# Kernel tuning notes

Hardware: AMD Instinct MI355X
Metric: run time of the kernel (lower is better)

## Reference

```python
import jax, jax.numpy as jnp
import numpy as np

NUM_CLUSTERS = 32
EPS = 1e-12

def _l2norm(v, axis):
    return v / jnp.maximum(jnp.linalg.norm(v, axis=axis, keepdims=True), EPS)

def setup_inputs() -> dict:
    key = jax.random.key(0)
    k1, k2, k3 = jax.random.split(key, 3)
    B, M, D, K = 64, 512, 2048, NUM_CLUSTERS
    init_sc = 1.0 / np.sqrt(D)
    x = jax.random.normal(k1, (B, M, D), dtype=jnp.float32)
    W = init_sc * jax.random.normal(k2, (K, D), dtype=jnp.float32)
    centroids = init_sc * jax.random.normal(k3, (K, D), dtype=jnp.float32)
    return {"x": x, "W": W, "centroids": centroids}

def reference(x, W, centroids):
    # x: [B, M, D] frame features; W: [K, D]; centroids: [K, D]
    xn = _l2norm(x, axis=-1)                              # per-frame L2 normalize
    sa = jax.nn.softmax(jnp.einsum('bmd,kd->bmk', xn, W), axis=-1)  # [B, M, K]
    # vlad[b,k,d] = sum_m sa[b,m,k] * (xn[b,m,d] - centroids[k,d])
    #            = (sa^T @ xn)[b,k,d] - colsum(sa)[b,k] * centroids[k,d]
    agg = jnp.einsum('bmk,bmd->bkd', sa, xn)              # [B, K, D]
    vlad = agg - jnp.sum(sa, axis=1)[..., None] * centroids[None]
    vlad = _l2norm(vlad, axis=2)                          # intra-normalize per cluster
    vlad = vlad.reshape(vlad.shape[0], -1)                # [B, K*D]
    return _l2norm(vlad, axis=1)
```

## Files before the change

kernel.cpp:

```cpp
#include <hip/hip_runtime.h>
#include <hip/hip_bf16.h>
#include <cstdint>
#include <cstddef>

#define Bn 64
#define Mn 512
#define Dn 2048
#define Kn 32
#define EPSF 1e-12f

typedef __attribute__((ext_vector_type(8))) __bf16 bf16x8;
typedef __attribute__((ext_vector_type(4))) __bf16 bf16x4;
typedef __attribute__((ext_vector_type(4))) float f32x4;

__global__ __launch_bounds__(256) void k0_prep(const float* __restrict__ W,
                                               __bf16* __restrict__ Wb,
                                               float* __restrict__ ssq) {
  int idx = blockIdx.x * 256 + threadIdx.x;
  if (idx < Kn * Dn) Wb[idx] = (__bf16)W[idx];
  if (idx < Bn * Kn) ssq[idx] = 0.f;
}

__global__ __launch_bounds__(256) void k1_logits(const float* __restrict__ x,
                                                 const __bf16* __restrict__ Wb,
                                                 float* __restrict__ logits,
                                                 float* __restrict__ invn) {
  int wv = threadIdx.x >> 6, lane = threadIdx.x & 63;
  int mr = lane & 15, q = lane >> 4;
  int row0 = (blockIdx.x * 4 + wv) * 16;
  const float* xp = x + (size_t)(row0 + mr) * Dn + q * 8;
  const __bf16* wp = Wb + (size_t)mr * Dn + q * 8;
  f32x4 acc0 = {0.f, 0.f, 0.f, 0.f};
  f32x4 acc1 = {0.f, 0.f, 0.f, 0.f};
  float ssq = 0.f;
#pragma unroll 2
  for (int s = 0; s < 64; ++s) {
    f32x4 xa = *(const f32x4*)(xp + s * 32);
    f32x4 xb = *(const f32x4*)(xp + s * 32 + 4);
    bf16x8 af;
    af[0] = (__bf16)xa[0]; af[1] = (__bf16)xa[1];
    af[2] = (__bf16)xa[2]; af[3] = (__bf16)xa[3];
    af[4] = (__bf16)xb[0]; af[5] = (__bf16)xb[1];
    af[6] = (__bf16)xb[2]; af[7] = (__bf16)xb[3];
    ssq = fmaf(xa[0], xa[0], ssq); ssq = fmaf(xa[1], xa[1], ssq);
    ssq = fmaf(xa[2], xa[2], ssq); ssq = fmaf(xa[3], xa[3], ssq);
    ssq = fmaf(xb[0], xb[0], ssq); ssq = fmaf(xb[1], xb[1], ssq);
    ssq = fmaf(xb[2], xb[2], ssq); ssq = fmaf(xb[3], xb[3], ssq);
    bf16x8 b0 = *(const bf16x8*)(wp + s * 32);
    bf16x8 b1 = *(const bf16x8*)(wp + (size_t)16 * Dn + s * 32);
    acc0 = __builtin_amdgcn_mfma_f32_16x16x32_bf16(af, b0, acc0, 0, 0, 0);
    acc1 = __builtin_amdgcn_mfma_f32_16x16x32_bf16(af, b1, acc1, 0, 0, 0);
  }
#pragma unroll
  for (int r = 0; r < 4; ++r) {
    int row = row0 + q * 4 + r;
    logits[(size_t)row * Kn + mr] = acc0[r];
    logits[(size_t)row * Kn + mr + 16] = acc1[r];
  }
  ssq += __shfl_xor(ssq, 16);
  ssq += __shfl_xor(ssq, 32);
  if (lane < 16) invn[row0 + lane] = 1.f / fmaxf(sqrtf(ssq), EPSF);
}

__global__ __launch_bounds__(512) void k2_softmax(const float* __restrict__ logits,
                                                  const float* __restrict__ invn,
                                                  __bf16* __restrict__ sapT,
                                                  float* __restrict__ colsum) {
  __shared__ float csw[8][Kn + 1];
  int b = blockIdx.x, t = threadIdx.x;
  int row = b * Mn + t;
  float inv = invn[row];
  const float* lp = logits + (size_t)row * Kn;
  float v[Kn];
#pragma unroll
  for (int k = 0; k < Kn; ++k) v[k] = lp[k] * inv;
  float mx = v[0];
#pragma unroll
  for (int k = 1; k < Kn; ++k) mx = fmaxf(mx, v[k]);
  float sum = 0.f;
#pragma unroll
  for (int k = 0; k < Kn; ++k) { v[k] = __expf(v[k] - mx); sum += v[k]; }
  float rs = 1.f / sum;
  __bf16* sp = sapT + (size_t)b * (Kn * Mn) + t;
#pragma unroll
  for (int k = 0; k < Kn; ++k) {
    v[k] *= rs;
    sp[(size_t)k * Mn] = (__bf16)(v[k] * inv);
  }
#pragma unroll
  for (int k = 0; k < Kn; ++k) {
#pragma unroll
    for (int off = 1; off <= 32; off <<= 1) v[k] += __shfl_xor(v[k], off);
  }
  int wv = t >> 6, lane = t & 63;
#pragma unroll
  for (int k = 0; k < Kn; ++k)
    if (lane == k) csw[wv][k] = v[k];
  __syncthreads();
  if (t < Kn) {
    float s = 0.f;
#pragma unroll
    for (int w = 0; w < 8; ++w) s += csw[w][t];
    colsum[b * Kn + t] = s;
  }
}

#define XS 36
#define AS 520
__global__ __launch_bounds__(256) void k3_agg(const float* __restrict__ x,
                                              const __bf16* __restrict__ sapT,
                                              const float* __restrict__ colsum,
                                              const float* __restrict__ cent,
                                              float* __restrict__ vlad,
                                              float* __restrict__ ssq) {
  __shared__ __bf16 xT[256 * XS];
  __shared__ __bf16 saT[Kn * AS];
  __shared__ float csl[Kn];
  int b = blockIdx.x >> 3;
  int dchunk = (blockIdx.x & 7) * 256;
  int t = threadIdx.x;
  {
    const __bf16* sg = sapT + (size_t)b * (Kn * Mn);
#pragma unroll
    for (int i = 0; i < 8; ++i) {
      int f = t + 256 * i;
      int k = f >> 6;
      int mg = (f & 63) * 8;
      *(bf16x8*)&saT[k * AS + mg] = *(const bf16x8*)(sg + k * Mn + mg);
    }
    if (t < Kn) csl[t] = colsum[b * Kn + t];
  }
  int w = t >> 6, lane = t & 63;
  int mr = lane & 15, q = lane >> 4;
  int r_ = t >> 3, qq = t & 7;
  const float* xg = x + (size_t)b * Mn * Dn + dchunk;
  f32x4 acc[2][4] = {};
  for (int m0 = 0; m0 < Mn; m0 += 32) {
    __syncthreads();
#pragma unroll
    for (int i = 0; i < 8; ++i) {
      int c0 = (qq + 8 * i) * 4;
      f32x4 xv = *(const f32x4*)(xg + (size_t)(m0 + r_) * Dn + c0);
      xT[(c0 + 0) * XS + r_] = (__bf16)xv[0];
      xT[(c0 + 1) * XS + r_] = (__bf16)xv[1];
      xT[(c0 + 2) * XS + r_] = (__bf16)xv[2];
      xT[(c0 + 3) * XS + r_] = (__bf16)xv[3];
    }
    __syncthreads();
    bf16x8 a0 = *(const bf16x8*)&saT[mr * AS + m0 + q * 8];
    bf16x8 a1 = *(const bf16x8*)&saT[(mr + 16) * AS + m0 + q * 8];
#pragma unroll
    for (int dt = 0; dt < 4; ++dt) {
      int c = w * 64 + dt * 16 + mr;
      bf16x4 lo = *(const bf16x4*)&xT[c * XS + q * 8];
      bf16x4 hi = *(const bf16x4*)&xT[c * XS + q * 8 + 4];
      bf16x8 bv = __builtin_shufflevector(lo, hi, 0, 1, 2, 3, 4, 5, 6, 7);
      acc[0][dt] = __builtin_amdgcn_mfma_f32_16x16x32_bf16(a0, bv, acc[0][dt], 0, 0, 0);
      acc[1][dt] = __builtin_amdgcn_mfma_f32_16x16x32_bf16(a1, bv, acc[1][dt], 0, 0, 0);
    }
  }
#pragma unroll
  for (int kt = 0; kt < 2; ++kt) {
#pragma unroll
    for (int r = 0; r < 4; ++r) {
      int kc = kt * 16 + q * 4 + r;
      float csv = csl[kc];
      float sqa = 0.f;
#pragma unroll
      for (int dt = 0; dt < 4; ++dt) {
        int col = dchunk + w * 64 + dt * 16 + mr;
        float vv = acc[kt][dt][r] - csv * cent[(size_t)kc * Dn + col];
        vlad[((size_t)(b * Kn + kc)) * Dn + col] = vv;
        sqa = fmaf(vv, vv, sqa);
      }
      sqa += __shfl_xor(sqa, 1); sqa += __shfl_xor(sqa, 2);
      sqa += __shfl_xor(sqa, 4); sqa += __shfl_xor(sqa, 8);
      if (mr == 0) atomicAdd(&ssq[b * Kn + kc], sqa);
    }
  }
}

__global__ __launch_bounds__(256) void k4_norm(float* __restrict__ out,
                                               const float* __restrict__ ssq) {
  __shared__ float rk[Kn];
  __shared__ float us[Kn];
  int b = blockIdx.x >> 4;
  int t = threadIdx.x;
  if (t < Kn) {
    float ss = ssq[b * Kn + t];
    float r = 1.f / fmaxf(sqrtf(ss), EPSF);
    rk[t] = r;
    us[t] = ss * r * r;
  }
  __syncthreads();
  float S = 0.f;
#pragma unroll
  for (int k = 0; k < Kn; ++k) S += us[k];
  float s = 1.f / fmaxf(sqrtf(S), EPSF);
  int chunk = blockIdx.x & 15;
  size_t base = (size_t)b * (Kn * Dn) + (size_t)chunk * 4096;
  f32x4* p = (f32x4*)(out + base);
#pragma unroll
  for (int i = 0; i < 4; ++i) {
    int idx = t + 256 * i;
    int k = (chunk * 4096 + idx * 4) >> 11;
    f32x4 v = p[idx];
    float sc = rk[k] * s;
    v[0] *= sc; v[1] *= sc; v[2] *= sc; v[3] *= sc;
    p[idx] = v;
  }
}

extern "C" void kernel_launch(void* const* d_in, const int* in_sizes, int n_in,
                              void* d_out, int out_size, void* d_ws, size_t ws_size,
                              hipStream_t stream) {
  const float* x = (const float*)d_in[0];
  const float* W = (const float*)d_in[1];
  const float* cent = (const float*)d_in[2];
  float* out = (float*)d_out;
  char* ws = (char*)d_ws;
  __bf16* Wb = (__bf16*)ws;
  float* invn = (float*)(ws + (131072));
  __bf16* sapT = (__bf16*)(ws + (262144));
  float* colsum = (float*)(ws + (262144 + 2097152));
  float* ssqb = (float*)(ws + (262144 + 2097152 + 8192));
  float* logits = out;
  hipLaunchKernelGGL(k0_prep, dim3(256), dim3(256), 0, stream, W, Wb, ssqb);
  hipLaunchKernelGGL(k1_logits, dim3(512), dim3(256), 0, stream, x, Wb, logits, invn);
  hipLaunchKernelGGL(k2_softmax, dim3(Bn), dim3(512), 0, stream, logits, invn, sapT, colsum);
  hipLaunchKernelGGL(k3_agg, dim3(512), dim3(256), 0, stream, x, sapT, colsum, cent, out, ssqb);
  hipLaunchKernelGGL(k4_norm, dim3(1024), dim3(256), 0, stream, out, ssqb);
}
```

Measured before the change: 452.7 us.

## Fuse softmax into logits kernel and rewrite aggregation as fp32 FMA

Softmax, its per-row normalization scaling and the cluster column sums now run inside the logits MFMA kernel using lane shuffles, with atomics for the column sums. This removes the separate softmax launch and the logits round-trip through global memory. The aggregation kernel drops the bf16 MFMA path, whose transpose into LDS used scattered bf16 stores. Instead each thread owns one feature column and accumulates 32 clusters with scalar fp32 FMAs against soft-assignment tiles broadcast from LDS. This trades matrix-core throughput and LDS reuse for plain vector ALU work with coalesced x reads, and adds more atomics.

```diff
diff --git a/kernel.cpp b/kernel.cpp
--- a/kernel.cpp
+++ b/kernel.cpp
@@ -10,24 +10,25 @@
 #define EPSF 1e-12f
 
 typedef __attribute__((ext_vector_type(8))) __bf16 bf16x8;
-typedef __attribute__((ext_vector_type(4))) __bf16 bf16x4;
 typedef __attribute__((ext_vector_type(4))) float f32x4;
 
 __global__ __launch_bounds__(256) void k0_prep(const float* __restrict__ W,
                                                __bf16* __restrict__ Wb,
+                                               float* __restrict__ colsum,
                                                float* __restrict__ ssq) {
   int idx = blockIdx.x * 256 + threadIdx.x;
   if (idx < Kn * Dn) Wb[idx] = (__bf16)W[idx];
-  if (idx < Bn * Kn) ssq[idx] = 0.f;
-}
-
-__global__ __launch_bounds__(256) void k1_logits(const float* __restrict__ x,
-                                                 const __bf16* __restrict__ Wb,
-                                                 float* __restrict__ logits,
-                                                 float* __restrict__ invn) {
+  if (idx < Bn * Kn) { colsum[idx] = 0.f; ssq[idx] = 0.f; }
+}
+
+__global__ __launch_bounds__(256) void k1_logits_softmax(const float* __restrict__ x,
+                                                         const __bf16* __restrict__ Wb,
+                                                         __bf16* __restrict__ saP,
+                                                         float* __restrict__ colsum) {
   int wv = threadIdx.x >> 6, lane = threadIdx.x & 63;
   int mr = lane & 15, q = lane >> 4;
   int row0 = (blockIdx.x * 4 + wv) * 16;
+  int b = row0 >> 9;
   const float* xp = x + (size_t)(row0 + mr) * Dn + q * 8;
   const __bf16* wp = Wb + (size_t)mr * Dn + q * 8;
   f32x4 acc0 = {0.f, 0.f, 0.f, 0.f};
@@ -51,132 +52,102 @@
     acc0 = __builtin_amdgcn_mfma_f32_16x16x32_bf16(af, b0, acc0, 0, 0, 0);
     acc1 = __builtin_amdgcn_mfma_f32_16x16x32_bf16(af, b1, acc1, 0, 0, 0);
   }
-#pragma unroll
-  for (int r = 0; r < 4; ++r) {
-    int row = row0 + q * 4 + r;
-    logits[(size_t)row * Kn + mr] = acc0[r];
-    logits[(size_t)row * Kn + mr + 16] = acc1[r];
-  }
   ssq += __shfl_xor(ssq, 16);
   ssq += __shfl_xor(ssq, 32);
-  if (lane < 16) invn[row0 + lane] = 1.f / fmaxf(sqrtf(ssq), EPSF);
-}
-
-__global__ __launch_bounds__(512) void k2_softmax(const float* __restrict__ logits,
-                                                  const float* __restrict__ invn,
-                                                  __bf16* __restrict__ sapT,
-                                                  float* __restrict__ colsum) {
-  __shared__ float csw[8][Kn + 1];
-  int b = blockIdx.x, t = threadIdx.x;
-  int row = b * Mn + t;
-  float inv = invn[row];
-  const float* lp = logits + (size_t)row * Kn;
-  float v[Kn];
-#pragma unroll
-  for (int k = 0; k < Kn; ++k) v[k] = lp[k] * inv;
-  float mx = v[0];
-#pragma unroll
-  for (int k = 1; k < Kn; ++k) mx = fmaxf(mx, v[k]);
-  float sum = 0.f;
-#pragma unroll
-  for (int k = 0; k < Kn; ++k) { v[k] = __expf(v[k] - mx); sum += v[k]; }
-  float rs = 1.f / sum;
-  __bf16* sp = sapT + (size_t)b * (Kn * Mn) + t;
-#pragma unroll
-  for (int k = 0; k < Kn; ++k) {
-    v[k] *= rs;
-    sp[(size_t)k * Mn] = (__bf16)(v[k] * inv);
-  }
-#pragma unroll
-  for (int k = 0; k < Kn; ++k) {
-#pragma unroll
-    for (int off = 1; off <= 32; off <<= 1) v[k] += __shfl_xor(v[k], off);
-  }
-  int wv = t >> 6, lane = t & 63;
-#pragma unroll
-  for (int k = 0; k < Kn; ++k)
-    if (lane == k) csw[wv][k] = v[k];
-  __syncthreads();
-  if (t < Kn) {
-    float s = 0.f;
-#pragma unroll
-    for (int w = 0; w < 8; ++w) s += csw[w][t];
-    colsum[b * Kn + t] = s;
-  }
-}
-
-#define XS 36
-#define AS 520
+  float invb = 1.f / fmaxf(sqrtf(ssq), EPSF);
+  float cs0 = 0.f, cs1 = 0.f;
+#pragma unroll
+  for (int r = 0; r < 4; ++r) {
+    float inv = __shfl(invb, q * 4 + r);
+    float v0 = acc0[r] * inv, v1 = acc1[r] * inv;
+    float mx = fmaxf(v0, v1);
+    mx = fmaxf(mx, __shfl_xor(mx, 1));
+    mx = fmaxf(mx, __shfl_xor(mx, 2));
+    mx = fmaxf(mx, __shfl_xor(mx, 4));
+    mx = fmaxf(mx, __shfl_xor(mx, 8));
+    float e0 = __expf(v0 - mx), e1 = __expf(v1 - mx);
+    float sm = e0 + e1;
+    sm += __shfl_xor(sm, 1); sm += __shfl_xor(sm, 2);
+    sm += __shfl_xor(sm, 4); sm += __shfl_xor(sm, 8);
+    float rs = 1.f / sm;
+    float sa0 = e0 * rs, sa1 = e1 * rs;
+    size_t ro = (size_t)(row0 + q * 4 + r) * Kn;
+    saP[ro + mr]      = (__bf16)(sa0 * inv);
+    saP[ro + mr + 16] = (__bf16)(sa1 * inv);
+    cs0 += sa0; cs1 += sa1;
+  }
+  cs0 += __shfl_xor(cs0, 16); cs0 += __shfl_xor(cs0, 32);
+  cs1 += __shfl_xor(cs1, 16); cs1 += __shfl_xor(cs1, 32);
+  if (lane < 16) {
+    atomicAdd(&colsum[b * Kn + mr], cs0);
+    atomicAdd(&colsum[b * Kn + mr + 16], cs1);
+  }
+}
+
+#define MT 128
 __global__ __launch_bounds__(256) void k3_agg(const float* __restrict__ x,
-                                              const __bf16* __restrict__ sapT,
+                                              const __bf16* __restrict__ saP,
                                               const float* __restrict__ colsum,
                                               const float* __restrict__ cent,
                                               float* __restrict__ vlad,
                                               float* __restrict__ ssq) {
-  __shared__ __bf16 xT[256 * XS];
-  __shared__ __bf16 saT[Kn * AS];
+  __shared__ float sa_t[MT * Kn];
   __shared__ float csl[Kn];
   int b = blockIdx.x >> 3;
-  int dchunk = (blockIdx.x & 7) * 256;
+  int d = (blockIdx.x & 7) * 256 + threadIdx.x;
   int t = threadIdx.x;
-  {
-    const __bf16* sg = sapT + (size_t)b * (Kn * Mn);
-#pragma unroll
-    for (int i = 0; i < 8; ++i) {
-      int f = t + 256 * i;
-      int k = f >> 6;
-      int mg = (f & 63) * 8;
-      *(bf16x8*)&saT[k * AS + mg] = *(const bf16x8*)(sg + k * Mn + mg);
-    }
-    if (t < Kn) csl[t] = colsum[b * Kn + t];
-  }
-  int w = t >> 6, lane = t & 63;
-  int mr = lane & 15, q = lane >> 4;
-  int r_ = t >> 3, qq = t & 7;
-  const float* xg = x + (size_t)b * Mn * Dn + dchunk;
-  f32x4 acc[2][4] = {};
-  for (int m0 = 0; m0 < Mn; m0 += 32) {
+  if (t < Kn) csl[t] = colsum[b * Kn + t];
+  float acc[Kn];
+#pragma unroll
+  for (int k = 0; k < Kn; ++k) acc[k] = 0.f;
+  const float* xb = x + (size_t)b * Mn * Dn + d;
+  const __bf16* sb = saP + (size_t)b * Mn * Kn;
+  for (int mt = 0; mt < Mn; mt += MT) {
     __syncthreads();
 #pragma unroll
-    for (int i = 0; i < 8; ++i) {
-      int c0 = (qq + 8 * i) * 4;
-      f32x4 xv = *(const f32x4*)(xg + (size_t)(m0 + r_) * Dn + c0);
-      xT[(c0 + 0) * XS + r_] = (__bf16)xv[0];
-      xT[(c0 + 1) * XS + r_] = (__bf16)xv[1];
-      xT[(c0 + 2) * XS + r_] = (__bf16)xv[2];
-      xT[(c0 + 3) * XS + r_] = (__bf16)xv[3];
+    for (int i = 0; i < 2; ++i) {
+      int u = t + 256 * i;
+      bf16x8 v8 = *(const bf16x8*)(sb + (size_t)(mt)*Kn + (size_t)u * 8);
+#pragma unroll
+      for (int j = 0; j < 8; ++j) sa_t[u * 8 + j] = (float)v8[j];
     }
     __syncthreads();
-    bf16x8 a0 = *(const bf16x8*)&saT[mr * AS + m0 + q * 8];
-    bf16x8 a1 = *(const bf16x8*)&saT[(mr + 16) * AS + m0 + q * 8];
-#pragma unroll
-    for (int dt = 0; dt < 4; ++dt) {
-      int c = w * 64 + dt * 16 + mr;
-      bf16x4 lo = *(const bf16x4*)&xT[c * XS + q * 8];
-      bf16x4 hi = *(const bf16x4*)&xT[c * XS + q * 8 + 4];
-      bf16x8 bv = __builtin_shufflevector(lo, hi, 0, 1, 2, 3, 4, 5, 6, 7);
-      acc[0][dt] = __builtin_amdgcn_mfma_f32_16x16x32_bf16(a0, bv, acc[0][dt], 0, 0, 0);
-      acc[1][dt] = __builtin_amdgcn_mfma_f32_16x16x32_bf16(a1, bv, acc[1][dt], 0, 0, 0);
+    const float* xp = xb + (size_t)mt * Dn;
+#pragma unroll 2
+    for (int mm = 0; mm < MT; mm += 4) {
+      float xv0 = xp[0];
+      float xv1 = xp[Dn];
+      float xv2 = xp[2 * Dn];
+      float xv3 = xp[3 * Dn];
+      xp += 4 * Dn;
+      const f32x4* sr0 = (const f32x4*)&sa_t[(mm + 0) * Kn];
+      const f32x4* sr1 = (const f32x4*)&sa_t[(mm + 1) * Kn];
+      const f32x4* sr2 = (const f32x4*)&sa_t[(mm + 2) * Kn];
+      const f32x4* sr3 = (const f32x4*)&sa_t[(mm + 3) * Kn];
+#pragma unroll
+      for (int g = 0; g < 8; ++g) {
+        f32x4 s0 = sr0[g], s1 = sr1[g], s2 = sr2[g], s3 = sr3[g];
+#pragma unroll
+        for (int c = 0; c < 4; ++c) {
+          int k = g * 4 + c;
+          acc[k] = fmaf(s0[c], xv0, acc[k]);
+          acc[k] = fmaf(s1[c], xv1, acc[k]);
+          acc[k] = fmaf(s2[c], xv2, acc[k]);
+          acc[k] = fmaf(s3[c], xv3, acc[k]);
+        }
+      }
     }
   }
-#pragma unroll
-  for (int kt = 0; kt < 2; ++kt) {
-#pragma unroll
-    for (int r = 0; r < 4; ++r) {
-      int kc = kt * 16 + q * 4 + r;
-      float csv = csl[kc];
-      float sqa = 0.f;
-#pragma unroll
-      for (int dt = 0; dt < 4; ++dt) {
-        int col = dchunk + w * 64 + dt * 16 + mr;
-        float vv = acc[kt][dt][r] - csv * cent[(size_t)kc * Dn + col];
-        vlad[((size_t)(b * Kn + kc)) * Dn + col] = vv;
-        sqa = fmaf(vv, vv, sqa);
-      }
-      sqa += __shfl_xor(sqa, 1); sqa += __shfl_xor(sqa, 2);
-      sqa += __shfl_xor(sqa, 4); sqa += __shfl_xor(sqa, 8);
-      if (mr == 0) atomicAdd(&ssq[b * Kn + kc], sqa);
-    }
+  int lane = t & 63;
+#pragma unroll
+  for (int k = 0; k < Kn; ++k) {
+    float vv = acc[k] - csl[k] * cent[(size_t)k * Dn + d];
+    vlad[((size_t)(b * Kn + k)) * Dn + d] = vv;
+    float sq = vv * vv;
+    sq += __shfl_xor(sq, 1);  sq += __shfl_xor(sq, 2);
+    sq += __shfl_xor(sq, 4);  sq += __shfl_xor(sq, 8);
+    sq += __shfl_xor(sq, 16); sq += __shfl_xor(sq, 32);
+    if (lane == 0) atomicAdd(&ssq[b * Kn + k], sq);
   }
 }
 
@@ -220,14 +191,11 @@
   float* out = (float*)d_out;
   char* ws = (char*)d_ws;
   __bf16* Wb = (__bf16*)ws;
-  float* invn = (float*)(ws + (131072));
-  __bf16* sapT = (__bf16*)(ws + (262144));
-  float* colsum = (float*)(ws + (262144 + 2097152));
-  float* ssqb = (float*)(ws + (262144 + 2097152 + 8192));
-  float* logits = out;
-  hipLaunchKernelGGL(k0_prep, dim3(256), dim3(256), 0, stream, W, Wb, ssqb);
-  hipLaunchKernelGGL(k1_logits, dim3(512), dim3(256), 0, stream, x, Wb, logits, invn);
-  hipLaunchKernelGGL(k2_softmax, dim3(Bn), dim3(512), 0, stream, logits, invn, sapT, colsum);
-  hipLaunchKernelGGL(k3_agg, dim3(512), dim3(256), 0, stream, x, sapT, colsum, cent, out, ssqb);
+  float* colsum = (float*)(ws + 131072);
+  float* ssqb = (float*)(ws + 131072 + 8192);
+  __bf16* saP = (__bf16*)(ws + 131072 + 16384);
+  hipLaunchKernelGGL(k0_prep, dim3(256), dim3(256), 0, stream, W, Wb, colsum, ssqb);
+  hipLaunchKernelGGL(k1_logits_softmax, dim3(512), dim3(256), 0, stream, x, Wb, saP, colsum);
+  hipLaunchKernelGGL(k3_agg, dim3(512), dim3(256), 0, stream, x, saP, colsum, cent, out, ssqb);
   hipLaunchKernelGGL(k4_norm, dim3(1024), dim3(256), 0, stream, out, ssqb);
 }
```

Result: slower. 498.4 us (+10.1%).
